# Optimization experiments

Measured on AMD Instinct MI355X. Metric: run time of the kernel, lower is better.

## Reference

```python
import jax, jax.numpy as jnp
from jax import lax
import numpy as np

N_BITS = 12
BATCH = 4_194_304


def setup_inputs() -> dict:
    key = jax.random.key(0)
    kA, kB = jax.random.split(key)
    # Binary spike inputs (0.0 / 1.0) as the SNN logic gates expect.
    A = jax.random.randint(kA, (BATCH, N_BITS), 0, 2).astype(jnp.float32)
    B = jax.random.randint(kB, (BATCH, N_BITS), 0, 2).astype(jnp.float32)
    return {"A": A, "B": B}


def reference(A, B):
    """12-bit ripple-borrow subtractor A - B using soft boolean gate algebra.

    Gate math on {0,1} spikes: XOR(a,b)=a+b-2ab, AND=ab, OR=a+b-ab, NOT=1-a.
    Bit 11 is the LSB (loop runs i=11..0), Bin defaults to 0.
    Returns (diff [..., 12], final_borrow [..., 1]).
    """

    def step(borrow, ab):  # borrow: [batch], a/b: [batch]
        a, b = ab
        t1 = a + b - 2.0 * a * b            # xor1: a ^ b
        diff = t1 + borrow - 2.0 * t1 * borrow  # xor2: t1 ^ borrow
        na = 1.0 - a                         # not a
        term1 = na * b                       # and1
        term2 = na * borrow                  # and2
        term3 = b * borrow                   # and3
        o1 = term1 + term2 - term1 * term2   # or1
        new_borrow = o1 + term3 - o1 * term3 # or2
        return new_borrow, diff

    # Reorder bits so scan walks LSB (index 11) -> MSB (index 0).
    a_seq = jnp.moveaxis(A, -1, 0)[::-1]  # [12, batch...]
    b_seq = jnp.moveaxis(B, -1, 0)[::-1]
    borrow0 = jnp.zeros_like(A[..., 0])

    borrow, diffs = lax.scan(step, borrow0, (a_seq, b_seq))
    diffs = jnp.moveaxis(diffs[::-1], 0, -1)  # back to [..., 12], index 0 = MSB
    return diffs, borrow[..., None]
```

## Files before the change

kernel.cpp:

```cpp
#include <hip/hip_runtime.h>


#define ROWS 256
#define LDS_STRIDE 13

__global__ __launch_bounds__(256) void Subtractor12Bit_kernel(
    const float4* __restrict__ A4,
    const float4* __restrict__ B4,
    float4* __restrict__ D4,
    float* __restrict__ Borrow,
    int batch)
{
    __shared__ float sa[ROWS * LDS_STRIDE];
    __shared__ float sb[ROWS * LDS_STRIDE];

    const int t = threadIdx.x;
    const int rowBase = blockIdx.x * ROWS;
    const int gbase = blockIdx.x * (ROWS * 3);

    const bool full = (rowBase + ROWS) <= batch;

    #pragma unroll
    for (int k = 0; k < 3; ++k) {
        const int f = t + 256 * k;
        const int r = f / 3;
        const int c = (f % 3) * 4;
        const int addr = r * LDS_STRIDE + c;
        if (full || (rowBase + r) < batch) {
            const float4 a = A4[gbase + f];
            const float4 b = B4[gbase + f];
            sa[addr + 0] = a.x; sa[addr + 1] = a.y; sa[addr + 2] = a.z; sa[addr + 3] = a.w;
            sb[addr + 0] = b.x; sb[addr + 1] = b.y; sb[addr + 2] = b.z; sb[addr + 3] = b.w;
        }
    }
    __syncthreads();

    const int row = rowBase + t;
    if (full || row < batch) {
        const int base = t * LDS_STRIDE;
        unsigned ua = 0u, ub = 0u;
        #pragma unroll
        for (int j = 0; j < 12; ++j) {
            ua |= (unsigned)(sa[base + j] > 0.5f) << (11 - j);
            ub |= (unsigned)(sb[base + j] > 0.5f) << (11 - j);
        }
        const unsigned diff = (ua - ub) & 0xFFFu;
        Borrow[row] = (ub > ua) ? 1.0f : 0.0f;
        #pragma unroll
        for (int j = 0; j < 12; ++j)
            sa[base + j] = (float)((diff >> (11 - j)) & 1u);
    }
    __syncthreads();

    #pragma unroll
    for (int k = 0; k < 3; ++k) {
        const int f = t + 256 * k;
        const int r = f / 3;
        const int c = (f % 3) * 4;
        const int addr = r * LDS_STRIDE + c;
        if (full || (rowBase + r) < batch) {
            float4 d;
            d.x = sa[addr + 0]; d.y = sa[addr + 1]; d.z = sa[addr + 2]; d.w = sa[addr + 3];
            D4[gbase + f] = d;
        }
    }
}

extern "C" void kernel_launch(void* const* d_in, const int* in_sizes, int n_in,
                              void* d_out, int out_size, void* d_ws, size_t ws_size,
                              hipStream_t stream) {
    const float* A = (const float*)d_in[0];
    const float* B = (const float*)d_in[1];
    float* out = (float*)d_out;

    const int batch = in_sizes[0] / 12;
    float* diffs = out;
    float* borrow = out + (size_t)batch * 12;

    const int grid = (batch + ROWS - 1) / ROWS;
    Subtractor12Bit_kernel<<<grid, 256, 0, stream>>>(
        (const float4*)A, (const float4*)B, (float4*)diffs, borrow, batch);
}
```

Before: 457.7 us.

## Replace LDS staging with direct per-row vector loads and grid-stride prefetch

Removes the shared-memory transpose: each thread loads its row's three 16-byte vectors directly, extracts bits via exponent-bit tests, and writes results as bit-masked 1.0f patterns with nontemporal stores. Uses a capped grid with grid-stride loop and software prefetch of the next row. Per-thread 48-byte strided loads are less coalesced per instruction than the prior layout, and the bit trick assumes inputs are exactly 0.0 or 1.0.

Measured after the change: 502.4 us. 9.8% more time.

```diff
diff --git a/kernel.cpp b/kernel.cpp
--- a/kernel.cpp
+++ b/kernel.cpp
@@ -1,83 +1,94 @@
 #include <hip/hip_runtime.h>
 
 
-#define ROWS 256
-#define LDS_STRIDE 13
+#define TPB  256
+#define NBLK 2048
 
-__global__ __launch_bounds__(256) void Subtractor12Bit_kernel(
-    const float4* __restrict__ A4,
-    const float4* __restrict__ B4,
-    float4* __restrict__ D4,
+typedef unsigned int uv4 __attribute__((ext_vector_type(4)));
+
+__device__ __forceinline__ unsigned pack12(const uv4& w0, const uv4& w1, const uv4& w2) {
+    unsigned p;
+    p  = ((w0.x >> 29) & 1u) << 11;
+    p |= ((w0.y >> 29) & 1u) << 10;
+    p |= ((w0.z >> 29) & 1u) << 9;
+    p |= ((w0.w >> 29) & 1u) << 8;
+    p |= ((w1.x >> 29) & 1u) << 7;
+    p |= ((w1.y >> 29) & 1u) << 6;
+    p |= ((w1.z >> 29) & 1u) << 5;
+    p |= ((w1.w >> 29) & 1u) << 4;
+    p |= ((w2.x >> 29) & 1u) << 3;
+    p |= ((w2.y >> 29) & 1u) << 2;
+    p |= ((w2.z >> 29) & 1u) << 1;
+    p |= ((w2.w >> 29) & 1u);
+    return p;
+}
+
+__device__ __forceinline__ unsigned bit2onef(unsigned diff, int k) {
+    return 0x3F800000u & (0u - ((diff >> k) & 1u));
+}
+
+__global__ __launch_bounds__(TPB) void Subtractor12Bit_kernel(
+    const uv4* __restrict__ A4,
+    const uv4* __restrict__ B4,
+    uv4* __restrict__ D4,
     float* __restrict__ Borrow,
     int batch)
 {
-    __shared__ float sa[ROWS * LDS_STRIDE];
-    __shared__ float sb[ROWS * LDS_STRIDE];
+    const int stride = gridDim.x * TPB;
+    int row = blockIdx.x * TPB + threadIdx.x;
+    if (row >= batch) return;
 
-    const int t = threadIdx.x;
-    const int rowBase = blockIdx.x * ROWS;
-    const int gbase = blockIdx.x * (ROWS * 3);
+    uv4 a0, a1, a2, b0, b1, b2;
+    {
+        const size_t base = (size_t)row * 3;
+        a0 = A4[base + 0]; a1 = A4[base + 1]; a2 = A4[base + 2];
+        b0 = B4[base + 0]; b1 = B4[base + 1]; b2 = B4[base + 2];
+    }
 
-    const bool full = (rowBase + ROWS) <= batch;
+    while (true) {
+        const int next = row + stride;
+        const bool have_next = next < batch;
 
-    #pragma unroll
-    for (int k = 0; k < 3; ++k) {
-        const int f = t + 256 * k;
-        const int r = f / 3;
-        const int c = (f % 3) * 4;
-        const int addr = r * LDS_STRIDE + c;
-        if (full || (rowBase + r) < batch) {
-            const float4 a = A4[gbase + f];
-            const float4 b = B4[gbase + f];
-            sa[addr + 0] = a.x; sa[addr + 1] = a.y; sa[addr + 2] = a.z; sa[addr + 3] = a.w;
-            sb[addr + 0] = b.x; sb[addr + 1] = b.y; sb[addr + 2] = b.z; sb[addr + 3] = b.w;
+        uv4 na0, na1, na2, nb0, nb1, nb2;
+        if (have_next) {
+            const size_t nb = (size_t)next * 3;
+            na0 = A4[nb + 0]; na1 = A4[nb + 1]; na2 = A4[nb + 2];
+            nb0 = B4[nb + 0]; nb1 = B4[nb + 1]; nb2 = B4[nb + 2];
         }
-    }
-    __syncthreads();
 
-    const int row = rowBase + t;
-    if (full || row < batch) {
-        const int base = t * LDS_STRIDE;
-        unsigned ua = 0u, ub = 0u;
-        #pragma unroll
-        for (int j = 0; j < 12; ++j) {
-            ua |= (unsigned)(sa[base + j] > 0.5f) << (11 - j);
-            ub |= (unsigned)(sb[base + j] > 0.5f) << (11 - j);
-        }
+        const unsigned ua = pack12(a0, a1, a2);
+        const unsigned ub = pack12(b0, b1, b2);
         const unsigned diff = (ua - ub) & 0xFFFu;
-        Borrow[row] = (ub > ua) ? 1.0f : 0.0f;
-        #pragma unroll
-        for (int j = 0; j < 12; ++j)
-            sa[base + j] = (float)((diff >> (11 - j)) & 1u);
-    }
-    __syncthreads();
 
-    #pragma unroll
-    for (int k = 0; k < 3; ++k) {
-        const int f = t + 256 * k;
-        const int r = f / 3;
-        const int c = (f % 3) * 4;
-        const int addr = r * LDS_STRIDE + c;
-        if (full || (rowBase + r) < batch) {
-            float4 d;
-            d.x = sa[addr + 0]; d.y = sa[addr + 1]; d.z = sa[addr + 2]; d.w = sa[addr + 3];
-            D4[gbase + f] = d;
-        }
+        uv4 d0 = {bit2onef(diff, 11), bit2onef(diff, 10), bit2onef(diff, 9), bit2onef(diff, 8)};
+        uv4 d1 = {bit2onef(diff, 7),  bit2onef(diff, 6),  bit2onef(diff, 5), bit2onef(diff, 4)};
+        uv4 d2 = {bit2onef(diff, 3),  bit2onef(diff, 2),  bit2onef(diff, 1), bit2onef(diff, 0)};
+
+        const size_t base = (size_t)row * 3;
+        __builtin_nontemporal_store(d0, &D4[base + 0]);
+        __builtin_nontemporal_store(d1, &D4[base + 1]);
+        __builtin_nontemporal_store(d2, &D4[base + 2]);
+        __builtin_nontemporal_store((ub > ua) ? 1.0f : 0.0f, &Borrow[row]);
+
+        if (!have_next) break;
+        a0 = na0; a1 = na1; a2 = na2;
+        b0 = nb0; b1 = nb1; b2 = nb2;
+        row = next;
     }
 }
 
 extern "C" void kernel_launch(void* const* d_in, const int* in_sizes, int n_in,
                               void* d_out, int out_size, void* d_ws, size_t ws_size,
                               hipStream_t stream) {
-    const float* A = (const float*)d_in[0];
-    const float* B = (const float*)d_in[1];
+    const uv4* A = (const uv4*)d_in[0];
+    const uv4* B = (const uv4*)d_in[1];
     float* out = (float*)d_out;
 
     const int batch = in_sizes[0] / 12;
-    float* diffs = out;
+    uv4* diffs = (uv4*)out;
     float* borrow = out + (size_t)batch * 12;
 
-    const int grid = (batch + ROWS - 1) / ROWS;
-    Subtractor12Bit_kernel<<<grid, 256, 0, stream>>>(
-        (const float4*)A, (const float4*)B, (float4*)diffs, borrow, batch);
+    int grid = (batch + TPB - 1) / TPB;
+    if (grid > NBLK) grid = NBLK;
+    Subtractor12Bit_kernel<<<grid, TPB, 0, stream>>>(A, B, diffs, borrow, batch);
 }
```
